# Kernel tuning notes

Measured on AMD Instinct MI355X. Metric: run time of the kernel, lower is better.

## Reference

```python
import jax, jax.numpy as jnp
import numpy as np

NUM_CAPS_OUT = 10
NUM_NODES = 32 * 6 * 6  # 1152
IN_DIM = 8
OUT_DIM = 16
ROUTING_ITERS = 3


def squash(x):
    # scale = |x|^2/(1+|x|^2); out = scale * x/|x|  (no epsilon, faithful to torch)
    sn = jnp.sum(x * x, axis=-1, keepdims=True)
    return sn / (1.0 + sn) * x / jnp.sqrt(sn)


def setup_inputs() -> dict:
    key = jax.random.key(0)
    ks = jax.random.split(key, 6)
    B = 512
    images = jax.random.normal(ks[0], (B, 1, 28, 28), dtype=jnp.float32)
    # ConvLayer: Conv2d(1, 256, k=9, s=1) with bias
    conv1_w = jax.random.normal(ks[1], (256, 1, 9, 9), dtype=jnp.float32) * 0.05
    conv1_b = jnp.zeros((256,), dtype=jnp.float32)
    prim_w = jax.random.normal(ks[2], (8 * 32, 256, 9, 9), dtype=jnp.float32) * 0.01
    prim_b = jnp.zeros((8 * 32,), dtype=jnp.float32)
    # DigitCaps weight: torch.randn(10, 1152, 8, 16)
    W = jax.random.normal(ks[3], (NUM_CAPS_OUT, NUM_NODES, IN_DIM, OUT_DIM), dtype=jnp.float32)
    return {"images": images, "conv1_w": conv1_w, "conv1_b": conv1_b,
            "prim_w": prim_w, "prim_b": prim_b, "W": W}


def reference(images, conv1_w, conv1_b, prim_w, prim_b, W):
    B = images.shape[0]
    dn = ('NCHW', 'OIHW', 'NCHW')
    # ConvLayer: 28x28 -> 20x20, 256 channels, ReLU
    x = jax.lax.conv_general_dilated(images, conv1_w, (1, 1), 'VALID', dimension_numbers=dn)
    x = jax.nn.relu(x + conv1_b[None, :, None, None])  # [B,256,20,20]
    # PrimaryCaps: 8 stacked convs -> [B, 8*32, 6, 6]; each capsule viewed as (32*6*6,)
    u = jax.lax.conv_general_dilated(x, prim_w, (2, 2), 'VALID', dimension_numbers=dn)
    u = u + prim_b[None, :, None, None]
    u = u.reshape(B, 8, NUM_NODES).transpose(0, 2, 1)  # [B,1152,8]
    u = squash(u)
    # DigitCaps: u_hat[c,b,n,o] = sum_i u[b,n,i] * W[c,n,i,o]
    u_hat = jnp.einsum('bni,cnio->cbno', u, W)  # [10,B,1152,16]
    # Dynamic routing (3 iterations). b_ij kept as [...,1]: torch replicates it
    # across the 16 out dims identically, so math is unchanged.
    b_ij = jnp.zeros(u_hat.shape[:-1] + (1,), dtype=u_hat.dtype)
    v_j = None
    for it in range(ROUTING_ITERS):
        c_ij = jax.nn.softmax(b_ij, axis=2)            # softmax over nodes
        s_j = jnp.sum(c_ij * u_hat, axis=2, keepdims=True)  # [10,B,1,16]
        v_j = squash(s_j)
        if it < ROUTING_ITERS - 1:
            a_ij = jnp.sum(u_hat * v_j, axis=-1, keepdims=True)  # [10,B,1152,1]
            b_ij = b_ij + a_ij
    # squeeze -> [10,B,16], transpose(0,1) -> [B,10,16]
    return v_j[:, :, 0, :].transpose(1, 0, 2)
```

## Files before the change

### kernel.cpp

```cpp
#include <hip/hip_runtime.h>
#include <hip/hip_bf16.h>
#include <cstddef>
#include <cstdint>

typedef __attribute__((ext_vector_type(8))) short v8s;
typedef __attribute__((ext_vector_type(16))) float v16f;

#define GLDS(SRC, DST) __builtin_amdgcn_global_load_lds( \
    (const __attribute__((address_space(1))) void*)(SRC), \
    (__attribute__((address_space(3))) void*)(DST), 16, 0, 0)

__device__ __forceinline__ void bf16split(float x, unsigned short& h, unsigned short& l) {
    union { float f; unsigned u; } a; a.f = x;
    unsigned r = a.u + 0x7fff + ((a.u >> 16) & 1);
    h = (unsigned short)(r >> 16);
    union { unsigned u; float f; } hb; hb.u = (unsigned)h << 16;
    union { float f; unsigned u; } b; b.f = x - hb.f;
    unsigned r2 = b.u + 0x7fff + ((b.u >> 16) & 1);
    l = (unsigned short)(r2 >> 16);
}

__global__ __launch_bounds__(256) void prep_kernel(
    const float* __restrict__ cw, const float* __restrict__ pw,
    float* __restrict__ wT1, char* __restrict__ wpk)
{
    int idx = blockIdx.x * 256 + threadIdx.x;
    if (idx < 81 * 256) {
        int k = idx >> 8, oc = idx & 255;
        wT1[idx] = cw[oc * 81 + k];
    }
    int Q = idx & 2047;
    int slab = idx >> 11;
    int D = Q << 4;
    int R = D >> 9;
    int v = (D & 511) ^ ((R & 31) << 4);
    int h = v >> 7, pl = (v >> 6) & 1, icb = v & 63;
    int ch = h * 64 + R;
    int g = slab / 81, k = slab - g * 81;
    int ic0 = g * 32 + (icb >> 1);
    const float* src = pw + ((size_t)ch * 256 + ic0) * 81 + k;
    v8s ov;
#pragma unroll
    for (int j = 0; j < 8; ++j) {
        unsigned short hh, ll; bf16split(src[(size_t)j * 81], hh, ll);
        ov[j] = (short)(pl ? ll : hh);
    }
    *(v8s*)(wpk + (size_t)slab * 32768 + D) = ov;
}

__global__ __launch_bounds__(256) void conv1_kernel(
    const float* __restrict__ img,
    const float* __restrict__ wT1,
    const float* __restrict__ bias,
    char* __restrict__ xc2,
    int b0)
{
    const int bl = blockIdx.x;
    const int oc = threadIdx.x;
    __shared__ __align__(16) float im[784];
    const float* ib = img + (size_t)(b0 + bl) * 784;
    for (int e = oc; e < 784; e += 256) im[e] = ib[e];
    float w[81];
#pragma unroll
    for (int k = 0; k < 81; ++k) w[k] = wT1[k * 256 + oc];
    float bv = bias[oc];
    __syncthreads();
    char* ob = xc2 + (size_t)bl * 409600;
    for (int oy = 0; oy < 20; ++oy) {
        float a[20];
#pragma unroll
        for (int ox = 0; ox < 20; ++ox) a[ox] = bv;
        for (int ky = 0; ky < 9; ++ky) {
            const float* rp = &im[(oy + ky) * 28];
            float r[28];
#pragma unroll
            for (int q = 0; q < 7; ++q) {
                float4 v4 = *(const float4*)(rp + q * 4);
                r[q * 4] = v4.x; r[q * 4 + 1] = v4.y;
                r[q * 4 + 2] = v4.z; r[q * 4 + 3] = v4.w;
            }
#pragma unroll
            for (int kx = 0; kx < 9; ++kx) {
                float wv = w[ky * 9 + kx];
#pragma unroll
                for (int ox = 0; ox < 20; ++ox)
                    a[ox] = fmaf(wv, r[ox + kx], a[ox]);
            }
        }
#pragma unroll
        for (int ox = 0; ox < 20; ++ox) {
            float av = fmaxf(a[ox], 0.f);
            unsigned short h, l; bf16split(av, h, l);
            char* rp2 = ob + (size_t)(oy * 20 + ox) * 1024;
            *(unsigned short*)(rp2 + oc * 2) = h;
            *(unsigned short*)(rp2 + 512 + oc * 2) = l;
        }
    }
}

__global__ __launch_bounds__(512, 1) void gemm_kernel(
    const char* __restrict__ xc2,
    const char* __restrict__ wpk,
    float* __restrict__ prim,
    int M, int Mtiles, int gm0)
{
    __shared__ __align__(128) char As[2][24576];
    __shared__ __align__(128) char Bs[2][32768];
    const int tid = threadIdx.x;
    const int w = tid >> 6, lane = tid & 63;
    const int wm = w & 1, wn = w >> 1;
    const int col = lane & 31, kg = lane >> 5;
    const int id = blockIdx.x;
    const int g = id / Mtiles;
    const int tile = id - g * Mtiles;
    const int m0 = tile * 192;

    int pbase[3], asrc[3];
#pragma unroll
    for (int i = 0; i < 3; ++i) {
        int d = (w * 3 + i) * 1024 + lane * 16;
        int R = d >> 9;
        int v = (d & 511) ^ ((R & 31) << 4);
        int h = v >> 7, pl = (v >> 6) & 1, icb = v & 63;
        int m = m0 + 48 * h + R; if (m >= M) m = M - 1;
        int b = m / 36, s6 = m - b * 36;
        pbase[i] = b * 400 + (s6 / 6) * 40 + (s6 % 6) * 2;
        asrc[i] = pl * 512 + g * 64 + icb;
    }
    int Abase[3], Ahof[3], Axor[3];
#pragma unroll
    for (int fm = 0; fm < 3; ++fm) {
        int m = wm * 96 + fm * 32 + col;
        int h = m / 48, R = m - h * 48;
        Abase[fm] = R * 512;
        Ahof[fm] = h * 128;
        Axor[fm] = (R & 31) << 4;
    }
    const char* wg = wpk + (size_t)g * 81 * 32768;

    v16f acc[3][2];
#pragma unroll
    for (int i = 0; i < 3; ++i)
#pragma unroll
        for (int j = 0; j < 2; ++j)
#pragma unroll
            for (int e = 0; e < 16; ++e) acc[i][j][e] = 0.f;

    auto stage = [&](int nb, int kk) {
        const int koff = (kk / 9) * 20 + (kk % 9);
#pragma unroll
        for (int i = 0; i < 3; ++i)
            GLDS(xc2 + (size_t)(pbase[i] + koff) * 1024 + asrc[i],
                 &As[nb][(w * 3 + i) * 1024]);
        const char* bs = wg + (size_t)kk * 32768;
#pragma unroll
        for (int i = 0; i < 4; ++i)
            GLDS(bs + (w * 4 + i) * 1024 + lane * 16,
                 &Bs[nb][(w * 4 + i) * 1024]);
    };

    stage(0, 0);
    __syncthreads();

    const int xr = col << 4;
    for (int k = 0; k < 81; ++k) {
        const int cur = k & 1;
        if (k < 80) stage(cur ^ 1, k + 1);
        const char* Ab = &As[cur][0];
        const char* Bb = &Bs[cur][0];
#pragma unroll
        for (int s = 0; s < 2; ++s) {
            const int vb = s * 32 + kg * 16;
            v8s Ah[3], Al[3], Bh[2], Bl[2];
#pragma unroll
            for (int fm = 0; fm < 3; ++fm) {
                const char* ap = Ab + Abase[fm];
                Ah[fm] = *(const v8s*)(ap + ((Ahof[fm] + vb) ^ Axor[fm]));
                Al[fm] = *(const v8s*)(ap + ((Ahof[fm] + 64 + vb) ^ Axor[fm]));
            }
#pragma unroll
            for (int fn = 0; fn < 2; ++fn) {
                const char* bp = Bb + (fn * 32 + col) * 512;
                Bh[fn] = *(const v8s*)(bp + ((wn * 128 + vb) ^ xr));
                Bl[fn] = *(const v8s*)(bp + ((wn * 128 + 64 + vb) ^ xr));
            }
            __builtin_amdgcn_s_setprio(1);
#pragma unroll
            for (int fn = 0; fn < 2; ++fn)
#pragma unroll
                for (int fm = 0; fm < 3; ++fm) {
                    acc[fm][fn] = __builtin_amdgcn_mfma_f32_32x32x16_bf16(Al[fm], Bh[fn], acc[fm][fn], 0, 0, 0);
                    acc[fm][fn] = __builtin_amdgcn_mfma_f32_32x32x16_bf16(Ah[fm], Bl[fn], acc[fm][fn], 0, 0, 0);
                    acc[fm][fn] = __builtin_amdgcn_mfma_f32_32x32x16_bf16(Ah[fm], Bh[fn], acc[fm][fn], 0, 0, 0);
                }
            __builtin_amdgcn_s_setprio(0);
        }
        if (k < 80) __syncthreads();
    }

    float* pg = prim + (size_t)gm0 * 256;
#pragma unroll
    for (int fm = 0; fm < 3; ++fm)
#pragma unroll
        for (int fn = 0; fn < 2; ++fn) {
            int ch = wn * 64 + fn * 32 + col;
#pragma unroll
            for (int rg = 0; rg < 16; ++rg) {
                int row = (rg & 3) + 8 * (rg >> 2) + 4 * kg;
                int m = m0 + wm * 96 + fm * 32 + row;
                if (m < M) atomicAdd(&pg[(size_t)m * 256 + ch], acc[fm][fn][rg]);
            }
        }
}

__global__ __launch_bounds__(256) void prim2u_kernel(
    const float* __restrict__ prim, const float* __restrict__ pb,
    float* __restrict__ u, int M)
{
    __shared__ float p[64 * 257];
    __shared__ float bsh[256];
    const int tid = threadIdx.x;
    const int rows0 = blockIdx.x * 64;
    bsh[tid] = pb[tid];
#pragma unroll
    for (int j = 0; j < 16; ++j) {
        int e4 = j * 256 + tid;
        int row = e4 >> 6, c4 = (e4 & 63) << 2;
        int rr = rows0 + row; if (rr >= M) rr = M - 1;
        float4 a = *(const float4*)(prim + (size_t)rr * 256 + c4);
        float* pp = &p[row * 257 + c4];
        pp[0] = a.x; pp[1] = a.y; pp[2] = a.z; pp[3] = a.w;
    }
    __syncthreads();
#pragma unroll
    for (int j = 0; j < 8; ++j) {
        int idx = j * 256 + tid;
        int row = idx & 63, cc = idx >> 6;
        int m = rows0 + row;
        if (m >= M) continue;
        int b = m / 36, s = m - b * 36;
        float p8[8]; float sn = 0.f;
#pragma unroll
        for (int d = 0; d < 8; ++d) {
            float v = p[row * 257 + d * 32 + cc] + bsh[d * 32 + cc];
            p8[d] = v; sn += v * v;
        }
        float fac = sqrtf(sn) / (1.0f + sn);
        float4 o0, o1;
        o0.x = fac * p8[0]; o0.y = fac * p8[1]; o0.z = fac * p8[2]; o0.w = fac * p8[3];
        o1.x = fac * p8[4]; o1.y = fac * p8[5]; o1.z = fac * p8[6]; o1.w = fac * p8[7];
        float* up = u + ((size_t)b * 1152 + cc * 36 + s) * 8;
        *(float4*)up = o0;
        *(float4*)(up + 4) = o1;
    }
}

__global__ __launch_bounds__(512) void routing_kernel(
    const float* __restrict__ u,
    const float* __restrict__ W,
    float* __restrict__ out,
    int B)
{
    const int b0 = blockIdx.x * 2;
    const int c = blockIdx.y;
    const int tid = threadIdx.x;
    __shared__ float uht[2][16][1152];
    __shared__ float bijs[2][1152];
    __shared__ float red[2][4 * 17];
    __shared__ float sred[2][17];
    __shared__ float mred[2][4];

    const float* __restrict__ Wc = W + (size_t)c * (1152 * 128);
    const int b1 = (b0 + 1 < B) ? b0 + 1 : b0;
    const float* __restrict__ ub0 = u + (size_t)b0 * 9216;
    const float* __restrict__ ub1 = u + (size_t)b1 * 9216;

    for (int n = tid; n < 1152; n += 512) {
        const float4* p0 = (const float4*)(ub0 + n * 8);
        const float4* p1 = (const float4*)(ub1 + n * 8);
        float4 a0 = p0[0], a1 = p0[1], c0 = p1[0], c1 = p1[1];
        float uu0[8] = {a0.x, a0.y, a0.z, a0.w, a1.x, a1.y, a1.z, a1.w};
        float uu1[8] = {c0.x, c0.y, c0.z, c0.w, c1.x, c1.y, c1.z, c1.w};
        float acc0[16], acc1[16];
#pragma unroll
        for (int o = 0; o < 16; ++o) { acc0[o] = 0.f; acc1[o] = 0.f; }
        const float* wn = Wc + n * 128;
#pragma unroll
        for (int i = 0; i < 8; ++i)
#pragma unroll
            for (int o = 0; o < 16; ++o) {
                float wv = wn[i * 16 + o];
                acc0[o] = fmaf(uu0[i], wv, acc0[o]);
                acc1[o] = fmaf(uu1[i], wv, acc1[o]);
            }
#pragma unroll
        for (int o = 0; o < 16; ++o) { uht[0][o][n] = acc0[o]; uht[1][o][n] = acc1[o]; }
        bijs[0][n] = 0.f; bijs[1][n] = 0.f;
    }
    __syncthreads();

    const int img = tid >> 8, t = tid & 255;
    const int wid = t >> 6, lane = t & 63;
    const float* __restrict__ UHT = &uht[img][0][0];
    float* __restrict__ bij = bijs[img];
    float* __restrict__ redi = red[img];
    float* __restrict__ sredi = sred[img];
    float* __restrict__ mredi = mred[img];

    float fac = 0.f, inv = 0.f;
    for (int it = 0; it < 3; ++it) {
        float m = -3.4e38f;
        for (int n = t; n < 1152; n += 256) m = fmaxf(m, bij[n]);
#pragma unroll
        for (int off = 32; off > 0; off >>= 1) m = fmaxf(m, __shfl_down(m, off));
        if (lane == 0) mredi[wid] = m;
        __syncthreads();
        float M = fmaxf(fmaxf(mredi[0], mredi[1]), fmaxf(mredi[2], mredi[3]));
        float se = 0.f;
        float sp[16];
#pragma unroll
        for (int o = 0; o < 16; ++o) sp[o] = 0.f;
        for (int n = t; n < 1152; n += 256) {
            float e = expf(bij[n] - M);
            se += e;
#pragma unroll
            for (int o = 0; o < 16; ++o) sp[o] = fmaf(e, UHT[o * 1152 + n], sp[o]);
        }
#pragma unroll
        for (int o = 0; o < 16; ++o)
#pragma unroll
            for (int off = 32; off > 0; off >>= 1) sp[o] += __shfl_down(sp[o], off);
#pragma unroll
        for (int off = 32; off > 0; off >>= 1) se += __shfl_down(se, off);
        if (lane == 0) {
#pragma unroll
            for (int o = 0; o < 16; ++o) redi[wid * 17 + o] = sp[o];
            redi[wid * 17 + 16] = se;
        }
        __syncthreads();
        if (t < 17)
            sredi[t] = redi[t] + redi[17 + t] + redi[34 + t] + redi[51 + t];
        __syncthreads();
        inv = 1.0f / sredi[16];
        float sn = 0.f;
        float sj[16];
#pragma unroll
        for (int o = 0; o < 16; ++o) { sj[o] = sredi[o] * inv; sn = fmaf(sj[o], sj[o], sn); }
        fac = sqrtf(sn) / (1.0f + sn);
        if (it < 2) {
            float v[16];
#pragma unroll
            for (int o = 0; o < 16; ++o) v[o] = fac * sj[o];
            for (int n = t; n < 1152; n += 256) {
                float a = 0.f;
#pragma unroll
                for (int o = 0; o < 16; ++o) a = fmaf(UHT[o * 1152 + n], v[o], a);
                bij[n] += a;
            }
        }
        __syncthreads();
    }
    if (t < 16 && b0 + img < B)
        out[((size_t)(b0 + img) * 10 + c) * 16 + t] = fac * (sredi[t] * inv);
}

extern "C" void kernel_launch(void* const* d_in, const int* in_sizes, int n_in,
                              void* d_out, int out_size, void* d_ws, size_t ws_size,
                              hipStream_t stream) {
    const float* images  = (const float*)d_in[0];
    const float* conv1_w = (const float*)d_in[1];
    const float* conv1_b = (const float*)d_in[2];
    const float* prim_w  = (const float*)d_in[3];
    const float* prim_b  = (const float*)d_in[4];
    const float* W       = (const float*)d_in[5];
    float* out = (float*)d_out;

    const int B = in_sizes[0] / 784;
    const int Mg = B * 36;
    const size_t usz = (size_t)B * 1152 * 8 * 4;
    const size_t xc2_full = (size_t)B * 409600;

    char* wsb = (char*)d_ws;
    size_t off = 0;
    float* wT1 = (float*)(wsb + off);
    off += 81 * 256 * 4;
    off = (off + 1023) & ~(size_t)1023;
    char* wpk = wsb + off;
    off += (size_t)648 * 32768;
    float* prim = (float*)(wsb + off);
    off += (size_t)Mg * 256 * 4;
    size_t rem = (ws_size > off) ? ws_size - off : 0;

    float* u;
    char* xc2base;
    int Bc;
    if (rem >= xc2_full) {
        xc2base = wsb + off;
        u = (float*)xc2base;
        Bc = B;
    } else {
        u = (float*)(wsb + off);
        off += usz;
        rem = (ws_size > off) ? ws_size - off : 0;
        xc2base = wsb + off;
        long Bcmax = (long)(rem / 409600);
        if (Bcmax < 1) Bcmax = 1;
        if (Bcmax > B) Bcmax = B;
        int nch = (int)((B + Bcmax - 1) / Bcmax);
        Bc = (B + nch - 1) / nch;
        Bc = (Bc + 15) & ~15;
        if (Bc > Bcmax) Bc = (int)(Bcmax & ~15L);
        if (Bc < 1) Bc = (int)Bcmax;
    }

    hipMemsetAsync(prim, 0, (size_t)Mg * 256 * 4, stream);
    prep_kernel<<<5184, 256, 0, stream>>>(conv1_w, prim_w, wT1, wpk);

    for (int b0 = 0; b0 < B; b0 += Bc) {
        int bc = (B - b0 < Bc) ? (B - b0) : Bc;
        conv1_kernel<<<bc, 256, 0, stream>>>(images, wT1, conv1_b, xc2base, b0);
        int M = bc * 36;
        int Mtiles = (M + 191) / 192;
        gemm_kernel<<<Mtiles * 8, 512, 0, stream>>>(xc2base, wpk, prim, M, Mtiles, b0 * 36);
    }
    prim2u_kernel<<<(Mg + 63) / 64, 256, 0, stream>>>(prim, prim_b, u, Mg);
    dim3 rg((B + 1) / 2, 10);
    routing_kernel<<<rg, 512, 0, stream>>>(u, W, out, B);
}
```

Measured before the change: 1.016 ms.

## Interleave prefetch loads with MFMA phases using explicit barriers in primary-caps GEMM

Splits each k-step of the primary-caps conv GEMM into four phases. Each phase issues a slice of the next tile's global-to-LDS loads, reads its fragments, then runs a group of MFMAs between s_barrier calls, with sched_barrier fences that stop the compiler from reordering. The aim is to spread memory traffic across the compute and keep waves in lockstep, replacing the bulk stage-then-syncthreads pattern. It adds extra barriers per k-step and relies on a manual vmcnt wait only before the final phase.

```diff
diff --git a/kernel.cpp b/kernel.cpp
--- a/kernel.cpp
+++ b/kernel.cpp
@@ -9,6 +9,9 @@
 #define GLDS(SRC, DST) __builtin_amdgcn_global_load_lds( \
     (const __attribute__((address_space(1))) void*)(SRC), \
     (__attribute__((address_space(3))) void*)(DST), 16, 0, 0)
+
+#define WAIT_VM0() asm volatile("s_waitcnt vmcnt(0)" ::: "memory")
+#define SCHED0()   __builtin_amdgcn_sched_barrier(0)
 
 __device__ __forceinline__ void bf16split(float x, unsigned short& h, unsigned short& l) {
     union { float f; unsigned u; } a; a.f = x;
@@ -146,56 +149,72 @@
 #pragma unroll
             for (int e = 0; e < 16; ++e) acc[i][j][e] = 0.f;
 
-    auto stage = [&](int nb, int kk) {
+    auto gldsA = [&](int nb, int kk, int i) {
         const int koff = (kk / 9) * 20 + (kk % 9);
-#pragma unroll
-        for (int i = 0; i < 3; ++i)
-            GLDS(xc2 + (size_t)(pbase[i] + koff) * 1024 + asrc[i],
-                 &As[nb][(w * 3 + i) * 1024]);
+        GLDS(xc2 + (size_t)(pbase[i] + koff) * 1024 + asrc[i],
+             &As[nb][(w * 3 + i) * 1024]);
+    };
+    auto gldsB = [&](int nb, int kk, int i) {
         const char* bs = wg + (size_t)kk * 32768;
-#pragma unroll
-        for (int i = 0; i < 4; ++i)
-            GLDS(bs + (w * 4 + i) * 1024 + lane * 16,
-                 &Bs[nb][(w * 4 + i) * 1024]);
+        GLDS(bs + (w * 4 + i) * 1024 + lane * 16,
+             &Bs[nb][(w * 4 + i) * 1024]);
     };
 
-    stage(0, 0);
-    __syncthreads();
+#pragma unroll
+    for (int i = 0; i < 3; ++i) gldsA(0, 0, i);
+#pragma unroll
+    for (int i = 0; i < 4; ++i) gldsB(0, 0, i);
+    WAIT_VM0(); SCHED0();
+    __builtin_amdgcn_s_barrier(); SCHED0();
 
     const int xr = col << 4;
     for (int k = 0; k < 81; ++k) {
-        const int cur = k & 1;
-        if (k < 80) stage(cur ^ 1, k + 1);
+        const int cur = k & 1, nxt = cur ^ 1;
+        const bool st = (k < 80);
         const char* Ab = &As[cur][0];
         const char* Bb = &Bs[cur][0];
-#pragma unroll
-        for (int s = 0; s < 2; ++s) {
+        v8s Ah[3], Al[3];
+
+#pragma unroll
+        for (int p = 0; p < 4; ++p) {
+            const int s = p >> 1, fn = p & 1;
             const int vb = s * 32 + kg * 16;
-            v8s Ah[3], Al[3], Bh[2], Bl[2];
+            if (st) {
+                if (p == 0) { gldsA(nxt, k + 1, 0); gldsA(nxt, k + 1, 1); }
+                else if (p == 1) { gldsA(nxt, k + 1, 2); gldsB(nxt, k + 1, 0); }
+                else if (p == 2) { gldsB(nxt, k + 1, 1); gldsB(nxt, k + 1, 2); }
+                else { gldsB(nxt, k + 1, 3); }
+            }
+            if (fn == 0) {
+#pragma unroll
+                for (int fm = 0; fm < 3; ++fm) {
+                    const char* ap = Ab + Abase[fm];
+                    Ah[fm] = *(const v8s*)(ap + ((Ahof[fm] + vb) ^ Axor[fm]));
+                    Al[fm] = *(const v8s*)(ap + ((Ahof[fm] + 64 + vb) ^ Axor[fm]));
+                }
+            }
+            const char* bp = Bb + (fn * 32 + col) * 512;
+            v8s Bh = *(const v8s*)(bp + ((wn * 128 + vb) ^ xr));
+            v8s Bl = *(const v8s*)(bp + ((wn * 128 + 64 + vb) ^ xr));
+
+            __builtin_amdgcn_s_barrier();
+            SCHED0();
+            __builtin_amdgcn_s_setprio(1);
 #pragma unroll
             for (int fm = 0; fm < 3; ++fm) {
-                const char* ap = Ab + Abase[fm];
-                Ah[fm] = *(const v8s*)(ap + ((Ahof[fm] + vb) ^ Axor[fm]));
-                Al[fm] = *(const v8s*)(ap + ((Ahof[fm] + 64 + vb) ^ Axor[fm]));
-            }
-#pragma unroll
-            for (int fn = 0; fn < 2; ++fn) {
-                const char* bp = Bb + (fn * 32 + col) * 512;
-                Bh[fn] = *(const v8s*)(bp + ((wn * 128 + vb) ^ xr));
-                Bl[fn] = *(const v8s*)(bp + ((wn * 128 + 64 + vb) ^ xr));
-            }
-            __builtin_amdgcn_s_setprio(1);
-#pragma unroll
-            for (int fn = 0; fn < 2; ++fn)
-#pragma unroll
-                for (int fm = 0; fm < 3; ++fm) {
-                    acc[fm][fn] = __builtin_amdgcn_mfma_f32_32x32x16_bf16(Al[fm], Bh[fn], acc[fm][fn], 0, 0, 0);
-                    acc[fm][fn] = __builtin_amdgcn_mfma_f32_32x32x16_bf16(Ah[fm], Bl[fn], acc[fm][fn], 0, 0, 0);
-                    acc[fm][fn] = __builtin_amdgcn_mfma_f32_32x32x16_bf16(Ah[fm], Bh[fn], acc[fm][fn], 0, 0, 0);
-                }
+                acc[fm][fn] = __builtin_amdgcn_mfma_f32_32x32x16_bf16(Al[fm], Bh, acc[fm][fn], 0, 0, 0);
+                acc[fm][fn] = __builtin_amdgcn_mfma_f32_32x32x16_bf16(Ah[fm], Bl, acc[fm][fn], 0, 0, 0);
+                acc[fm][fn] = __builtin_amdgcn_mfma_f32_32x32x16_bf16(Ah[fm], Bh, acc[fm][fn], 0, 0, 0);
+            }
             __builtin_amdgcn_s_setprio(0);
-        }
-        if (k < 80) __syncthreads();
+            SCHED0();
+            if (p < 3) {
+                __builtin_amdgcn_s_barrier();
+            } else if (st) {
+                WAIT_VM0(); SCHED0();
+                __builtin_amdgcn_s_barrier(); SCHED0();
+            }
+        }
     }
 
     float* pg = prim + (size_t)gm0 * 256;
```

Result: slower. 1.190 ms (+17.1%).
